# Performance work log

Hardware: AMD Instinct MI355X
Metric: run time of the kernel (lower is better)

## Reference

```python
import jax, jax.numpy as jnp
import numpy as np

B, L, D = 1, 1024, 128
EPS = 1e-5


def setup_inputs() -> dict:
    key = jax.random.key(0)
    ks = jax.random.split(key, 10)
    s = 1.0 / np.sqrt(D)
    return {
        "x": jax.random.normal(ks[0], (B, L, D), dtype=jnp.float32),
        "mask": jax.random.randint(ks[1], (B, L, L), 0, 2, dtype=jnp.int32),
        # JCrossOutProduct.l : Linear(D, D)
        "Wl": jax.random.uniform(ks[2], (D, D), jnp.float32, -s, s),
        "bl": jax.random.uniform(ks[3], (D,), jnp.float32, -s, s),
        # JCrossOutProduct.lo : Linear(D, D)
        "Wlo": jax.random.uniform(ks[4], (D, D), jnp.float32, -s, s),
        "blo": jax.random.uniform(ks[5], (D,), jnp.float32, -s, s),
        # JResCOPAttn.l : Linear(D, D)
        "Wl2": jax.random.uniform(ks[6], (D, D), jnp.float32, -s, s),
        "bl2": jax.random.uniform(ks[7], (D,), jnp.float32, -s, s),
        # LayerNorm(D)
        "gamma": jnp.ones((D,), jnp.float32),
        "beta": jnp.zeros((D,), jnp.float32),
    }


def reference(x, mask, Wl, bl, Wlo, blo, Wl2, bl2, gamma, beta):
    # a = self.cop.l(x) : [B, L, D]
    a = x @ Wl.T + bl
    # outer product kept per-channel: [B, L, L, D]
    outer = jnp.einsum('blc,bmc->blmc', a, a)
    # self.cop.lo over last dim: [B, L, L, D]
    tm = outer @ Wlo.T + blo
    # masked_fill(mask.unsqueeze(-1) == 0, 0.0)
    tm = tm * (mask[..., None] != 0).astype(tm.dtype)
    # tx = self.l(x)
    tx = x @ Wl2.T + bl2
    # per-channel attention-like contraction: out[b,c,d] = sum_a tm[b,c,a,d] * tx[b,a,d]
    y = x + jnp.einsum('bcad,bad->bcd', tm, tx)
    # shadow (eval): Dropout=identity, activator 'none'=identity, LayerNorm(D)
    mu = jnp.mean(y, axis=-1, keepdims=True)
    var = jnp.mean(jnp.square(y - mu), axis=-1, keepdims=True)
    return (y - mu) * jax.lax.rsqrt(var + EPS) * gamma + beta
```

## Files before the change

kernel.cpp:

```cpp
#include <hip/hip_runtime.h>
#include <hip/hip_fp16.h>


typedef _Float16 f16x8 __attribute__((ext_vector_type(8)));
typedef float    f32x4 __attribute__((ext_vector_type(4)));
typedef unsigned int       u32;
typedef unsigned long long u64;

#define LL   1024
#define DD   128
#define MCH  64
#define TPAD 66
#define EPSV 1e-5f

__global__ __launch_bounds__(256) void prep_kernel(
    const float* __restrict__ x,  const float* __restrict__ Wl,
    const float* __restrict__ bl, const float* __restrict__ Wlo,
    const float* __restrict__ Wl2,const float* __restrict__ bl2,
    _Float16* __restrict__ a_h, float* __restrict__ tx_out,
    _Float16* __restrict__ wh)
{
    __shared__ float xs[16*128];
    __shared__ float wsh[64*129];
    const int t  = threadIdx.x;
    const int bx = blockIdx.x;
    const int by = blockIdx.y;
    const int l0 = by*16;

    #pragma unroll
    for (int i = 0; i < 8; ++i) { int f = i*256 + t; xs[f] = x[l0*DD + f]; }
    const float* Wsrc = ((bx < 2) ? Wl : Wl2) + (bx & 1)*64*DD;
    #pragma unroll
    for (int i = 0; i < 32; ++i) {
        int f = i*256 + t; int r = f >> 7, k = f & 127;
        wsh[r*129 + k] = Wsrc[f];
    }
    __syncthreads();

    const int col  = t & 63;
    const int lsub = t >> 6;
    const float4* X4 = (const float4*)xs;
    float acc0 = 0.f, acc1 = 0.f, acc2 = 0.f, acc3 = 0.f;
    #pragma unroll
    for (int k4 = 0; k4 < 32; ++k4) {
        const float* wp = wsh + col*129 + k4*4;
        float4 wv = {wp[0], wp[1], wp[2], wp[3]};
        float4 x0 = X4[(lsub*4+0)*32 + k4];
        float4 x1 = X4[(lsub*4+1)*32 + k4];
        float4 x2 = X4[(lsub*4+2)*32 + k4];
        float4 x3 = X4[(lsub*4+3)*32 + k4];
        acc0 += wv.x*x0.x + wv.y*x0.y + wv.z*x0.z + wv.w*x0.w;
        acc1 += wv.x*x1.x + wv.y*x1.y + wv.z*x1.z + wv.w*x1.w;
        acc2 += wv.x*x2.x + wv.y*x2.y + wv.z*x2.z + wv.w*x2.w;
        acc3 += wv.x*x3.x + wv.y*x3.y + wv.z*x3.z + wv.w*x3.w;
    }
    const int colg = (bx & 1)*64 + col;
    const float bv = ((bx < 2) ? bl : bl2)[colg];
    if (bx < 2) {
        a_h[(l0+lsub*4+0)*DD + colg] = (_Float16)(acc0 + bv);
        a_h[(l0+lsub*4+1)*DD + colg] = (_Float16)(acc1 + bv);
        a_h[(l0+lsub*4+2)*DD + colg] = (_Float16)(acc2 + bv);
        a_h[(l0+lsub*4+3)*DD + colg] = (_Float16)(acc3 + bv);
    } else {
        tx_out[(l0+lsub*4+0)*DD + colg] = acc0 + bv;
        tx_out[(l0+lsub*4+1)*DD + colg] = acc1 + bv;
        tx_out[(l0+lsub*4+2)*DD + colg] = acc2 + bv;
        tx_out[(l0+lsub*4+3)*DD + colg] = acc3 + bv;
    }

    const int gid = (by*4 + bx)*256 + t;
    if (gid < DD*DD) wh[gid] = (_Float16)Wlo[gid];
}

#define COMPUTE(MI, AM, TV, WM)                                               \
  do {                                                                        \
    f16x8 ah_[2];                                                             \
    ah_[0] = al[0] * (AM)[0];                                                 \
    ah_[1] = al[1] * (AM)[1];                                                 \
    f32x4 c_[4];                                                              \
    _Pragma("unroll")                                                         \
    for (int nf_ = 0; nf_ < 4; ++nf_)                                         \
      c_[nf_] = f32x4{blov[nf_], blov[nf_], blov[nf_], blov[nf_]};            \
    _Pragma("unroll")                                                         \
    for (int kf_ = 0; kf_ < 2; ++kf_) {                                       \
      c_[0] = __builtin_amdgcn_mfma_f32_16x16x32_f16(ah_[kf_], bh[0][kf_], c_[0],0,0,0); \
      c_[1] = __builtin_amdgcn_mfma_f32_16x16x32_f16(ah_[kf_], bh[1][kf_], c_[1],0,0,0); \
      c_[2] = __builtin_amdgcn_mfma_f32_16x16x32_f16(ah_[kf_], bh[2][kf_], c_[2],0,0,0); \
      c_[3] = __builtin_amdgcn_mfma_f32_16x16x32_f16(ah_[kf_], bh[3][kf_], c_[3],0,0,0); \
    }                                                                         \
    _Pragma("unroll")                                                         \
    for (int r_ = 0; r_ < 4; ++r_) {                                          \
      const bool on_ = (((WM)[r_] >> (MI)) & 1u) != 0;                        \
      _Pragma("unroll")                                                       \
      for (int nf_ = 0; nf_ < 4; ++nf_)                                       \
        y[nf_][r_] = fmaf(on_ ? (TV)[nf_] : 0.0f, c_[nf_][r_], y[nf_][r_]);   \
    }                                                                         \
  } while (0)

#define HALF_LOOP(WM, MOFF)                                                   \
  for (int ms = 0; ms < 32; ms += 2) {                                        \
    f16x8 am0[2], am1[2];                                                     \
    am0[0] = *(const f16x8*)(ash + (MOFF + ms)*DD     + kbase + 0*32 + grp*8);\
    am0[1] = *(const f16x8*)(ash + (MOFF + ms)*DD     + kbase + 1*32 + grp*8);\
    am1[0] = *(const f16x8*)(ash + (MOFF + ms + 1)*DD + kbase + 0*32 + grp*8);\
    am1[1] = *(const f16x8*)(ash + (MOFF + ms + 1)*DD + kbase + 1*32 + grp*8);\
    float tvA[4], tvB[4];                                                     \
    _Pragma("unroll")                                                         \
    for (int nf = 0; nf < 4; ++nf) {                                          \
      float2 f2 = __half22float2(                                             \
          *(const __half2*)(txt + (dbase + nf*16 + ln)*TPAD + MOFF + ms));    \
      tvA[nf] = f2.x; tvB[nf] = f2.y;                                         \
    }                                                                         \
    COMPUTE(ms,     am0, tvA, WM);                                            \
    COMPUTE(ms + 1, am1, tvB, WM);                                            \
  }

__global__ __launch_bounds__(512, 4) void heavy_kernel(
    const _Float16* __restrict__ a_h, const float* __restrict__ tx,
    const _Float16* __restrict__ wh,  const int* __restrict__ mask,
    const float* __restrict__ blo,    _Float16* __restrict__ part)
{
    __shared__ __align__(16) _Float16 ash[MCH*DD];
    __shared__ __align__(4)  _Float16 txt[DD*TPAD];
    __shared__ u64 mbits[32];
    const int t     = threadIdx.x;
    const int lane  = t & 63, w = t >> 6;
    const int chunk = blockIdx.x;
    const int ltile = blockIdx.y;
    const int l0 = ltile*32, m0 = chunk*MCH;

    {
        const float4* s4 = (const float4*)(a_h + m0*DD);
        float4* d4 = (float4*)ash;
        #pragma unroll
        for (int i = 0; i < 2; ++i) d4[i*512 + t] = s4[i*512 + t];
    }
    {
        #pragma unroll
        for (int i = 0; i < 4; ++i) {
            int idx = i*512 + t;
            int m = idx >> 5, dg = idx & 31;
            float4 v = *(const float4*)(tx + (m0+m)*DD + dg*4);
            txt[(dg*4+0)*TPAD + m] = (_Float16)v.x;
            txt[(dg*4+1)*TPAD + m] = (_Float16)v.y;
            txt[(dg*4+2)*TPAD + m] = (_Float16)v.z;
            txt[(dg*4+3)*TPAD + m] = (_Float16)v.w;
        }
    }
    {
        #pragma unroll
        for (int i = 0; i < 4; ++i) {
            int idx = i*512 + t;
            int row = idx >> 6, mcol = idx & 63;
            u64 b = __ballot(mask[(l0 + row)*LL + m0 + mcol] != 0);
            if ((t & 63) == 0) mbits[row] = b;
        }
    }
    __syncthreads();

    const int grp = lane >> 4, ln = lane & 15;
    const int wl = w >> 2, wd = (w >> 1) & 1, kh = w & 1;
    const int lbase = l0 + wl*16;
    const int dbase = wd*64;
    const int kbase = kh*64;

    f16x8 bh[4][2];
    #pragma unroll
    for (int nf = 0; nf < 4; ++nf)
        #pragma unroll
        for (int kf = 0; kf < 2; ++kf)
            bh[nf][kf] = *(const f16x8*)(wh + (dbase + nf*16 + ln)*DD
                                            + kbase + kf*32 + grp*8);

    f16x8 al[2];
    #pragma unroll
    for (int kf = 0; kf < 2; ++kf)
        al[kf] = *(const f16x8*)(a_h + (lbase + ln)*DD + kbase + kf*32 + grp*8);

    float blov[4];
    if (kh == 0) {
        #pragma unroll
        for (int nf = 0; nf < 4; ++nf) blov[nf] = blo[dbase + nf*16 + ln];
    } else {
        #pragma unroll
        for (int nf = 0; nf < 4; ++nf) blov[nf] = 0.0f;
    }

    const int lrow0 = wl*16 + grp*4;
    u32 wmbL[4], wmbH[4];
    #pragma unroll
    for (int r = 0; r < 4; ++r) {
        u64 b = mbits[lrow0 + r];
        wmbL[r] = (u32)b; wmbH[r] = (u32)(b >> 32);
    }

    f32x4 y[4] = {{0,0,0,0},{0,0,0,0},{0,0,0,0},{0,0,0,0}};

    HALF_LOOP(wmbL, 0);
    HALF_LOOP(wmbH, 32);

    _Float16* dst = part + (size_t)(chunk*2 + kh)*(LL*DD);
    const int mrow0 = lbase + grp*4;
    #pragma unroll
    for (int nf = 0; nf < 4; ++nf)
        #pragma unroll
        for (int r = 0; r < 4; ++r)
            dst[(mrow0 + r)*DD + dbase + nf*16 + ln] = (_Float16)y[nf][r];
}

__global__ __launch_bounds__(128) void finish_kernel(
    const float* __restrict__ x, const _Float16* __restrict__ part,
    const float* __restrict__ gamma, const float* __restrict__ beta,
    float* __restrict__ out)
{
    const int l = blockIdx.x, t = threadIdx.x;
    float v = x[l*DD + t];
    #pragma unroll
    for (int ch = 0; ch < 32; ++ch)
        v += (float)part[((size_t)ch*LL + l)*DD + t];

    float s = v, s2 = v*v;
    #pragma unroll
    for (int o = 32; o > 0; o >>= 1) {
        s  += __shfl_xor(s, o);
        s2 += __shfl_xor(s2, o);
    }
    __shared__ float red[4];
    if ((t & 63) == 0) { red[(t>>6)*2+0] = s; red[(t>>6)*2+1] = s2; }
    __syncthreads();
    const float S  = red[0] + red[2];
    const float S2 = red[1] + red[3];
    const float mu  = S * (1.0f/128.0f);
    const float var = S2 * (1.0f/128.0f) - mu*mu;
    const float inv = rsqrtf(var + EPSV);
    out[l*DD + t] = (v - mu)*inv*gamma[t] + beta[t];
}

extern "C" void kernel_launch(void* const* d_in, const int* in_sizes, int n_in,
                              void* d_out, int out_size, void* d_ws, size_t ws_size,
                              hipStream_t stream)
{
    (void)in_sizes; (void)n_in; (void)out_size; (void)ws_size;
    const float* x     = (const float*)d_in[0];
    const int*   mask  = (const int*)  d_in[1];
    const float* Wl    = (const float*)d_in[2];
    const float* bl    = (const float*)d_in[3];
    const float* Wlo   = (const float*)d_in[4];
    const float* blo   = (const float*)d_in[5];
    const float* Wl2   = (const float*)d_in[6];
    const float* bl2   = (const float*)d_in[7];
    const float* gamma = (const float*)d_in[8];
    const float* beta  = (const float*)d_in[9];
    float* out = (float*)d_out;

    char* ws = (char*)d_ws;
    _Float16* a_h  = (_Float16*)(ws);
    float*    tx_b = (float*)   (ws + (256u<<10));
    _Float16* wh   = (_Float16*)(ws + (768u<<10));
    _Float16* part = (_Float16*)(ws + (1024u<<10));

    prep_kernel  <<<dim3(4,64),  256, 0, stream>>>(x, Wl, bl, Wlo, Wl2, bl2,
                                                   a_h, tx_b, wh);
    heavy_kernel <<<dim3(16,32), 512, 0, stream>>>(a_h, tx_b, wh, mask, blo, part);
    finish_kernel<<<1024, 128, 0, stream>>>(x, part, gamma, beta, out);
}
```

Measured before the change: 137.0 us.

## Fold mask and tx into MFMA operands, accumulating across m inside the matrix unit

The heavy kernel no longer runs a separate MFMA per m row and then does a scalar masked FMA into y. It scales the Wlo fragments by tx[m,d] and zeroes the A operand when the mask is off, so the sum over m happens inside the MFMA accumulator. The bias term is handled by one small mask-by-tx MFMA at the end. Each wave now covers the full K=128, which removes the k-split, halves the partial buffers that the finish kernel reads, and stores tx row-major with no transpose. The costs are extra f16 vector multiplies per iteration, f16 rounding of the tx*W product, and a lower occupancy hint in launch bounds.

```diff
diff --git a/kernel.cpp b/kernel.cpp
--- a/kernel.cpp
+++ b/kernel.cpp
@@ -3,6 +3,7 @@
 
 
 typedef _Float16 f16x8 __attribute__((ext_vector_type(8)));
+typedef _Float16 f16x2 __attribute__((ext_vector_type(2)));
 typedef float    f32x4 __attribute__((ext_vector_type(4)));
 typedef unsigned int       u32;
 typedef unsigned long long u64;
@@ -10,7 +11,6 @@
 #define LL   1024
 #define DD   128
 #define MCH  64
-#define TPAD 66
 #define EPSV 1e-5f
 
 __global__ __launch_bounds__(256) void prep_kernel(
@@ -72,56 +72,44 @@
     if (gid < DD*DD) wh[gid] = (_Float16)Wlo[gid];
 }
 
-#define COMPUTE(MI, AM, TV, WM)                                               \
+#define MITER(MI, WM, MOFF)                                                   \
   do {                                                                        \
-    f16x8 ah_[2];                                                             \
-    ah_[0] = al[0] * (AM)[0];                                                 \
-    ah_[1] = al[1] * (AM)[1];                                                 \
-    f32x4 c_[4];                                                              \
-    _Pragma("unroll")                                                         \
-    for (int nf_ = 0; nf_ < 4; ++nf_)                                         \
-      c_[nf_] = f32x4{blov[nf_], blov[nf_], blov[nf_], blov[nf_]};            \
-    _Pragma("unroll")                                                         \
-    for (int kf_ = 0; kf_ < 2; ++kf_) {                                       \
-      c_[0] = __builtin_amdgcn_mfma_f32_16x16x32_f16(ah_[kf_], bh[0][kf_], c_[0],0,0,0); \
-      c_[1] = __builtin_amdgcn_mfma_f32_16x16x32_f16(ah_[kf_], bh[1][kf_], c_[1],0,0,0); \
-      c_[2] = __builtin_amdgcn_mfma_f32_16x16x32_f16(ah_[kf_], bh[2][kf_], c_[2],0,0,0); \
-      c_[3] = __builtin_amdgcn_mfma_f32_16x16x32_f16(ah_[kf_], bh[3][kf_], c_[3],0,0,0); \
-    }                                                                         \
-    _Pragma("unroll")                                                         \
-    for (int r_ = 0; r_ < 4; ++r_) {                                          \
-      const bool on_ = (((WM)[r_] >> (MI)) & 1u) != 0;                        \
-      _Pragma("unroll")                                                       \
-      for (int nf_ = 0; nf_ < 4; ++nf_)                                       \
-        y[nf_][r_] = fmaf(on_ ? (TV)[nf_] : 0.0f, c_[nf_][r_], y[nf_][r_]);   \
-    }                                                                         \
+    const int mg_ = (MOFF) + (MI);                                            \
+    f16x8 am0_ = *(const f16x8*)(ash + mg_*DD + 0*32 + grp*8);                \
+    f16x8 am1_ = *(const f16x8*)(ash + mg_*DD + 1*32 + grp*8);                \
+    f16x8 am2_ = *(const f16x8*)(ash + mg_*DD + 2*32 + grp*8);                \
+    f16x8 am3_ = *(const f16x8*)(ash + mg_*DD + 3*32 + grp*8);                \
+    _Float16 h0_ = txf[mg_*DD + dbase + ln];                                  \
+    _Float16 h1_ = txf[mg_*DD + dbase + 16 + ln];                             \
+    const bool on_ = (((WM) >> (MI)) & 1u) != 0;                              \
+    f16x8 z_ = {};                                                            \
+    f16x8 ah0_ = on_ ? al[0]*am0_ : z_;                                       \
+    f16x8 ah1_ = on_ ? al[1]*am1_ : z_;                                       \
+    f16x8 ah2_ = on_ ? al[2]*am2_ : z_;                                       \
+    f16x8 ah3_ = on_ ? al[3]*am3_ : z_;                                       \
+    f16x8 s0_ = {h0_,h0_,h0_,h0_,h0_,h0_,h0_,h0_};                            \
+    f16x8 s1_ = {h1_,h1_,h1_,h1_,h1_,h1_,h1_,h1_};                            \
+    f16x8 b00_ = bh[0][0]*s0_, b01_ = bh[0][1]*s0_;                           \
+    f16x8 b02_ = bh[0][2]*s0_, b03_ = bh[0][3]*s0_;                           \
+    f16x8 b10_ = bh[1][0]*s1_, b11_ = bh[1][1]*s1_;                           \
+    f16x8 b12_ = bh[1][2]*s1_, b13_ = bh[1][3]*s1_;                           \
+    c0 = __builtin_amdgcn_mfma_f32_16x16x32_f16(ah0_, b00_, c0, 0,0,0);       \
+    c1 = __builtin_amdgcn_mfma_f32_16x16x32_f16(ah0_, b10_, c1, 0,0,0);       \
+    c0 = __builtin_amdgcn_mfma_f32_16x16x32_f16(ah1_, b01_, c0, 0,0,0);       \
+    c1 = __builtin_amdgcn_mfma_f32_16x16x32_f16(ah1_, b11_, c1, 0,0,0);       \
+    c0 = __builtin_amdgcn_mfma_f32_16x16x32_f16(ah2_, b02_, c0, 0,0,0);       \
+    c1 = __builtin_amdgcn_mfma_f32_16x16x32_f16(ah2_, b12_, c1, 0,0,0);       \
+    c0 = __builtin_amdgcn_mfma_f32_16x16x32_f16(ah3_, b03_, c0, 0,0,0);       \
+    c1 = __builtin_amdgcn_mfma_f32_16x16x32_f16(ah3_, b13_, c1, 0,0,0);       \
   } while (0)
 
-#define HALF_LOOP(WM, MOFF)                                                   \
-  for (int ms = 0; ms < 32; ms += 2) {                                        \
-    f16x8 am0[2], am1[2];                                                     \
-    am0[0] = *(const f16x8*)(ash + (MOFF + ms)*DD     + kbase + 0*32 + grp*8);\
-    am0[1] = *(const f16x8*)(ash + (MOFF + ms)*DD     + kbase + 1*32 + grp*8);\
-    am1[0] = *(const f16x8*)(ash + (MOFF + ms + 1)*DD + kbase + 0*32 + grp*8);\
-    am1[1] = *(const f16x8*)(ash + (MOFF + ms + 1)*DD + kbase + 1*32 + grp*8);\
-    float tvA[4], tvB[4];                                                     \
-    _Pragma("unroll")                                                         \
-    for (int nf = 0; nf < 4; ++nf) {                                          \
-      float2 f2 = __half22float2(                                             \
-          *(const __half2*)(txt + (dbase + nf*16 + ln)*TPAD + MOFF + ms));    \
-      tvA[nf] = f2.x; tvB[nf] = f2.y;                                         \
-    }                                                                         \
-    COMPUTE(ms,     am0, tvA, WM);                                            \
-    COMPUTE(ms + 1, am1, tvB, WM);                                            \
-  }
-
-__global__ __launch_bounds__(512, 4) void heavy_kernel(
+__global__ __launch_bounds__(512, 2) void heavy_kernel(
     const _Float16* __restrict__ a_h, const float* __restrict__ tx,
     const _Float16* __restrict__ wh,  const int* __restrict__ mask,
     const float* __restrict__ blo,    _Float16* __restrict__ part)
 {
     __shared__ __align__(16) _Float16 ash[MCH*DD];
-    __shared__ __align__(4)  _Float16 txt[DD*TPAD];
+    __shared__ __align__(16) _Float16 txf[MCH*DD];
     __shared__ u64 mbits[32];
     const int t     = threadIdx.x;
     const int lane  = t & 63, w = t >> 6;
@@ -141,10 +129,10 @@
             int idx = i*512 + t;
             int m = idx >> 5, dg = idx & 31;
             float4 v = *(const float4*)(tx + (m0+m)*DD + dg*4);
-            txt[(dg*4+0)*TPAD + m] = (_Float16)v.x;
-            txt[(dg*4+1)*TPAD + m] = (_Float16)v.y;
-            txt[(dg*4+2)*TPAD + m] = (_Float16)v.z;
-            txt[(dg*4+3)*TPAD + m] = (_Float16)v.w;
+            f16x2 p0 = {(_Float16)v.x, (_Float16)v.y};
+            f16x2 p1 = {(_Float16)v.z, (_Float16)v.w};
+            *(f16x2*)(txf + m*DD + dg*4)     = p0;
+            *(f16x2*)(txf + m*DD + dg*4 + 2) = p1;
         }
     }
     {
@@ -159,53 +147,62 @@
     __syncthreads();
 
     const int grp = lane >> 4, ln = lane & 15;
-    const int wl = w >> 2, wd = (w >> 1) & 1, kh = w & 1;
+    const int wl = w >> 2, wq = w & 3;
     const int lbase = l0 + wl*16;
-    const int dbase = wd*64;
-    const int kbase = kh*64;
-
-    f16x8 bh[4][2];
-    #pragma unroll
-    for (int nf = 0; nf < 4; ++nf)
+    const int dbase = wq*32;
+
+    f16x8 bh[2][4];
+    #pragma unroll
+    for (int nf = 0; nf < 2; ++nf)
+        #pragma unroll
+        for (int kf = 0; kf < 4; ++kf)
+            bh[nf][kf] = *(const f16x8*)(wh + (dbase + nf*16 + ln)*DD
+                                            + kf*32 + grp*8);
+
+    f16x8 al[4];
+    #pragma unroll
+    for (int kf = 0; kf < 4; ++kf)
+        al[kf] = *(const f16x8*)(a_h + (lbase + ln)*DD + kf*32 + grp*8);
+
+    const u64 mw = mbits[wl*16 + ln];
+    const u32 mwL = (u32)mw, mwH = (u32)(mw >> 32);
+
+    f32x4 c0 = {0,0,0,0}, c1 = {0,0,0,0};
+
+    #pragma unroll 2
+    for (int ms = 0; ms < 32; ++ms) MITER(ms, mwL, 0);
+    #pragma unroll 2
+    for (int ms = 0; ms < 32; ++ms) MITER(ms, mwH, 32);
+
+    f16x8 a2[2];
+    #pragma unroll
+    for (int kf = 0; kf < 2; ++kf)
+        #pragma unroll
+        for (int j = 0; j < 8; ++j)
+            a2[kf][j] = (_Float16)(int)((mw >> (kf*32 + grp*8 + j)) & 1ull);
+    f16x8 b2[2][2];
+    #pragma unroll
+    for (int nf = 0; nf < 2; ++nf)
         #pragma unroll
         for (int kf = 0; kf < 2; ++kf)
-            bh[nf][kf] = *(const f16x8*)(wh + (dbase + nf*16 + ln)*DD
-                                            + kbase + kf*32 + grp*8);
-
-    f16x8 al[2];
-    #pragma unroll
-    for (int kf = 0; kf < 2; ++kf)
-        al[kf] = *(const f16x8*)(a_h + (lbase + ln)*DD + kbase + kf*32 + grp*8);
-
-    float blov[4];
-    if (kh == 0) {
-        #pragma unroll
-        for (int nf = 0; nf < 4; ++nf) blov[nf] = blo[dbase + nf*16 + ln];
-    } else {
-        #pragma unroll
-        for (int nf = 0; nf < 4; ++nf) blov[nf] = 0.0f;
-    }
-
-    const int lrow0 = wl*16 + grp*4;
-    u32 wmbL[4], wmbH[4];
+            #pragma unroll
+            for (int j = 0; j < 8; ++j)
+                b2[nf][kf][j] = txf[(kf*32 + grp*8 + j)*DD + dbase + nf*16 + ln];
+    f32x4 s0 = {0,0,0,0}, s1 = {0,0,0,0};
+    s0 = __builtin_amdgcn_mfma_f32_16x16x32_f16(a2[0], b2[0][0], s0, 0,0,0);
+    s0 = __builtin_amdgcn_mfma_f32_16x16x32_f16(a2[1], b2[0][1], s0, 0,0,0);
+    s1 = __builtin_amdgcn_mfma_f32_16x16x32_f16(a2[0], b2[1][0], s1, 0,0,0);
+    s1 = __builtin_amdgcn_mfma_f32_16x16x32_f16(a2[1], b2[1][1], s1, 0,0,0);
+
+    const float blov0 = blo[dbase + ln];
+    const float blov1 = blo[dbase + 16 + ln];
+    _Float16* dst = part + (size_t)chunk*(LL*DD);
+    const int mrow0 = lbase + grp*4;
     #pragma unroll
     for (int r = 0; r < 4; ++r) {
-        u64 b = mbits[lrow0 + r];
-        wmbL[r] = (u32)b; wmbH[r] = (u32)(b >> 32);
-    }
-
-    f32x4 y[4] = {{0,0,0,0},{0,0,0,0},{0,0,0,0},{0,0,0,0}};
-
-    HALF_LOOP(wmbL, 0);
-    HALF_LOOP(wmbH, 32);
-
-    _Float16* dst = part + (size_t)(chunk*2 + kh)*(LL*DD);
-    const int mrow0 = lbase + grp*4;
-    #pragma unroll
-    for (int nf = 0; nf < 4; ++nf)
-        #pragma unroll
-        for (int r = 0; r < 4; ++r)
-            dst[(mrow0 + r)*DD + dbase + nf*16 + ln] = (_Float16)y[nf][r];
+        dst[(mrow0 + r)*DD + dbase + ln]      = (_Float16)fmaf(blov0, s0[r], c0[r]);
+        dst[(mrow0 + r)*DD + dbase + 16 + ln] = (_Float16)fmaf(blov1, s1[r], c1[r]);
+    }
 }
 
 __global__ __launch_bounds__(128) void finish_kernel(
@@ -216,7 +213,7 @@
     const int l = blockIdx.x, t = threadIdx.x;
     float v = x[l*DD + t];
     #pragma unroll
-    for (int ch = 0; ch < 32; ++ch)
+    for (int ch = 0; ch < 16; ++ch)
         v += (float)part[((size_t)ch*LL + l)*DD + t];
 
     float s = v, s2 = v*v;
```

Result: faster. 129.1 us (-5.8%).
